# Performance work log

Measured on AMD Instinct MI355X. Metric: run time of the kernel, lower is better.

## Reference

```python
import jax, jax.numpy as jnp
import numpy as np

DN = ('NCDHW', 'OIDHW', 'NCDHW')  # torch Conv3d layout

def conv3d(x, w, b, pad):
    y = jax.lax.conv_general_dilated(x, w, (1, 1, 1), [(p, p) for p in pad], dimension_numbers=DN)
    return y + b[None, :, None, None, None]

def setup_inputs() -> dict:
    key = jax.random.key(0)
    ks = jax.random.split(key, 10)
    C, Cq = 64, 8  # in_channels, in_channels // 8
    s = 0.05
    x = jax.random.normal(ks[0], (2, C, 16, 16, 16), dtype=jnp.float32)
    return {
        'x': x,
        'wq': jax.random.normal(ks[1], (Cq, C, 1, 3, 1), jnp.float32) * s,
        'bq': jax.random.normal(ks[2], (Cq,), jnp.float32) * s,
        'wk': jax.random.normal(ks[3], (Cq, C, 3, 1, 1), jnp.float32) * s,
        'bk': jax.random.normal(ks[4], (Cq,), jnp.float32) * s,
        'wj': jax.random.normal(ks[5], (Cq, C, 1, 1, 3), jnp.float32) * s,
        'bj': jax.random.normal(ks[6], (Cq,), jnp.float32) * s,
        'wv': jax.random.normal(ks[7], (C, C, 1, 1, 1), jnp.float32) * s,
        'bv': jax.random.normal(ks[8], (C,), jnp.float32) * s,
        'gamma': jax.random.normal(ks[9], (1,), jnp.float32) * s,
    }

def reference(x, wq, bq, wk, bk, wj, bj, wv, bv, gamma):
    B, C, H, W, D = x.shape
    N = H * W * D
    q = conv3d(x, wq, bq, (0, 1, 0)).reshape(B, -1, N)   # [B, c, N]
    k = conv3d(x, wk, bk, (1, 0, 0)).reshape(B, -1, N)   # [B, c, N]
    j = conv3d(x, wj, bj, (0, 0, 1)).reshape(B, -1, N)   # [B, c, N]
    # affinity = (Q^T K) (J^T K) reassociated as Q^T (K J^T) K  -- identical math,
    # O(N^2 c) instead of O(N^3) since c = C//8 << N.
    kj = jnp.einsum('bcn,bdn->bcd', k, j)                # [B, c, c] = K @ J^T
    aff = jnp.einsum('bcn,bcd,bdm->bnm', q, kj, k)       # [B, N, N]
    aff = jax.nn.softmax(aff, axis=-1)
    v = conv3d(x, wv, bv, (0, 0, 0)).reshape(B, C, N)    # [B, C, N]
    weights = jnp.einsum('bcn,bnm->bcm', v, aff).reshape(B, C, H, W, D)
    return gamma * weights + x
```

## Files before the change

### kernel.cpp

```cpp
#include <hip/hip_runtime.h>

#define N 4096
#define CIN 64
#define NB 2

typedef unsigned short u16;
typedef short bf16x8 __attribute__((ext_vector_type(8)));
typedef float f32x4 __attribute__((ext_vector_type(4)));

#define OFF_QT 0
#define OFF_KT (OFF_QT + NB*N*8)
#define OFF_JT (OFF_KT + NB*N*8)
#define OFF_V  (OFF_JT + NB*N*8)
#define OFF_QK (OFF_V + NB*CIN*N)
#define OFF_MX (OFF_QK + NB*N*8)
#define OFF_SC (OFF_MX + NB*N)

__device__ __forceinline__ u16 f2bf(float f) {
    union { float f; unsigned u; } v; v.f = f;
    unsigned r = (v.u + 0x7fffu + ((v.u >> 16) & 1u)) >> 16;
    return (u16)r;
}

__global__ __launch_bounds__(256) void prep(
        const float* __restrict__ x,
        const float* __restrict__ wq, const float* __restrict__ bq,
        const float* __restrict__ wk, const float* __restrict__ bk,
        const float* __restrict__ wj, const float* __restrict__ bj,
        const float* __restrict__ wv, const float* __restrict__ bv,
        float* __restrict__ ws, u16* __restrict__ vbf, float* __restrict__ out) {
    int n = blockIdx.x * 256 + threadIdx.x;
    int y = blockIdx.y;
    int b = blockIdx.z;
    const float* xb = x + (size_t)b * CIN * N + n;

    if (y < 8) {
        int cq = y;
        int d = n & 15, w = (n >> 4) & 15, h = n >> 8;
        int owl = (w > 0) ? -16 : 0,  owh = (w < 15) ? 16 : 0;
        int ohl = (h > 0) ? -256 : 0, ohh = (h < 15) ? 256 : 0;
        int odl = (d > 0) ? -1 : 0,   odh = (d < 15) ? 1 : 0;
        float mwl = (w > 0) ? 1.f : 0.f, mwh = (w < 15) ? 1.f : 0.f;
        float mhl = (h > 0) ? 1.f : 0.f, mhh = (h < 15) ? 1.f : 0.f;
        float mdl = (d > 0) ? 1.f : 0.f, mdh = (d < 15) ? 1.f : 0.f;
        float q = bq[cq], k = bk[cq], j = bj[cq];
        for (int c0 = 0; c0 < CIN; c0 += 8) {
            float xc[8], xwl[8], xwh[8], xhl[8], xhh[8], xdl[8], xdh[8];
#pragma unroll
            for (int u = 0; u < 8; ++u) {
                const float* p = xb + (size_t)(c0 + u) * N;
                xc[u]  = p[0];
                xwl[u] = p[owl]; xwh[u] = p[owh];
                xhl[u] = p[ohl]; xhh[u] = p[ohh];
                xdl[u] = p[odl]; xdh[u] = p[odh];
            }
#pragma unroll
            for (int u = 0; u < 8; ++u) {
                int c = c0 + u;
                const float* wqr = wq + (cq * CIN + c) * 3;
                const float* wkr = wk + (cq * CIN + c) * 3;
                const float* wjr = wj + (cq * CIN + c) * 3;
                q += wqr[0] * (xwl[u] * mwl) + wqr[1] * xc[u] + wqr[2] * (xwh[u] * mwh);
                k += wkr[0] * (xhl[u] * mhl) + wkr[1] * xc[u] + wkr[2] * (xhh[u] * mhh);
                j += wjr[0] * (xdl[u] * mdl) + wjr[1] * xc[u] + wjr[2] * (xdh[u] * mdh);
            }
        }
        size_t base = (size_t)(b * N + n) * 8 + cq;
        ws[OFF_QT + base] = q;
        ws[OFF_KT + base] = k;
        ws[OFF_JT + base] = j;
    } else {
        int yy = y - 8;
        int co0 = yy * 8;
        float acc[8];
#pragma unroll
        for (int i = 0; i < 8; ++i) acc[i] = bv[co0 + i];
        for (int c0 = 0; c0 < CIN; c0 += 8) {
            float xv[8];
#pragma unroll
            for (int u = 0; u < 8; ++u) xv[u] = xb[(size_t)(c0 + u) * N];
#pragma unroll
            for (int u = 0; u < 8; ++u)
#pragma unroll
                for (int i = 0; i < 8; ++i)
                    acc[i] += wv[(co0 + i) * CIN + c0 + u] * xv[u];
            if ((c0 >> 3) == yy) {
#pragma unroll
                for (int u = 0; u < 8; ++u)
                    out[(size_t)(b * CIN + c0 + u) * N + n] = xv[u];
            }
        }
#pragma unroll
        for (int i = 0; i < 8; ++i)
            vbf[(size_t)(b * CIN + co0 + i) * N + n] = f2bf(acc[i]);
    }
}

__global__ __launch_bounds__(256) void kjqkj(const float* __restrict__ ws_in,
                                             float* __restrict__ ws) {
    __shared__ float kjpart[4][64];
    __shared__ float kjs[64];
    const int t = threadIdx.x, lane = t & 63, wid = t >> 6;
    const int b = blockIdx.y;
    const float* ktb = ws_in + OFF_KT + (size_t)b * N * 8;
    const float* jtb = ws_in + OFF_JT + (size_t)b * N * 8;
    const float* qtb = ws_in + OFF_QT + (size_t)b * N * 8;

    float acc[64];
#pragma unroll
    for (int i = 0; i < 64; ++i) acc[i] = 0.f;
    for (int i = 0; i < 16; ++i) {
        int nn = i * 256 + t;
        const float4* kt = (const float4*)(ktb + (size_t)nn * 8);
        const float4* jt = (const float4*)(jtb + (size_t)nn * 8);
        float4 ka = kt[0], kb = kt[1], ja = jt[0], jb = jt[1];
        float kv[8] = {ka.x, ka.y, ka.z, ka.w, kb.x, kb.y, kb.z, kb.w};
        float jv[8] = {ja.x, ja.y, ja.z, ja.w, jb.x, jb.y, jb.z, jb.w};
#pragma unroll
        for (int c = 0; c < 8; ++c)
#pragma unroll
            for (int dd = 0; dd < 8; ++dd) acc[c * 8 + dd] += kv[c] * jv[dd];
    }
#pragma unroll
    for (int s = 32; s >= 1; s >>= 1)
#pragma unroll
        for (int i = 0; i < 64; ++i) acc[i] += __shfl_down(acc[i], s, 64);
    if (lane == 0) {
#pragma unroll
        for (int i = 0; i < 64; ++i) kjpart[wid][i] = acc[i];
    }
    __syncthreads();
    if (t < 64) kjs[t] = kjpart[0][t] + kjpart[1][t] + kjpart[2][t] + kjpart[3][t];
    __syncthreads();

    float kjr[64];
#pragma unroll
    for (int i = 0; i < 64; ++i) kjr[i] = kjs[i];
    int m = blockIdx.x * 256 + t;
    const float4* qt = (const float4*)(qtb + (size_t)m * 8);
    float4 qa = qt[0], qb = qt[1];
    float qv[8] = {qa.x, qa.y, qa.z, qa.w, qb.x, qb.y, qb.z, qb.w};
    float o[8];
#pragma unroll
    for (int dd = 0; dd < 8; ++dd) {
        float a = 0.f;
#pragma unroll
        for (int c = 0; c < 8; ++c) a += qv[c] * kjr[c * 8 + dd];
        o[dd] = a;
    }
    float4* dst = (float4*)(ws + OFF_QK + (size_t)(b * N + m) * 8);
    dst[0] = make_float4(o[0], o[1], o[2], o[3]);
    dst[1] = make_float4(o[4], o[5], o[6], o[7]);
}

__global__ __launch_bounds__(256) void pass1(const float* __restrict__ ws,
                                             float* __restrict__ mx_o, float* __restrict__ sc_o,
                                             const float* __restrict__ gamma) {
    int wid = threadIdx.x >> 6, lane = threadIdx.x & 63;
    int gw = blockIdx.x * 4 + wid;
    int r0 = gw * 4;
    int b = r0 >> 12;
    float4 qa[4], qb[4];
#pragma unroll
    for (int rr = 0; rr < 4; ++rr) {
        const float4* q4 = (const float4*)(ws + OFF_QK + (size_t)(r0 + rr) * 8);
        qa[rr] = q4[0]; qb[rr] = q4[1];
    }
    const float* ktb = ws + OFF_KT + (size_t)b * N * 8;
    float mx[4], sm[4];
#pragma unroll
    for (int rr = 0; rr < 4; ++rr) { mx[rr] = -3.0e38f; sm[rr] = 0.f; }
#pragma unroll 4
    for (int i = 0; i < 64; ++i) {
        int m = i * 64 + lane;
        const float4* kk4 = (const float4*)(ktb + (size_t)m * 8);
        float4 ka = kk4[0], kb = kk4[1];
#pragma unroll
        for (int rr = 0; rr < 4; ++rr) {
            float a = qa[rr].x * ka.x + qa[rr].y * ka.y + qa[rr].z * ka.z + qa[rr].w * ka.w
                    + qb[rr].x * kb.x + qb[rr].y * kb.y + qb[rr].z * kb.z + qb[rr].w * kb.w;
            float nm = fmaxf(mx[rr], a);
            sm[rr] = sm[rr] * __expf(mx[rr] - nm) + __expf(a - nm);
            mx[rr] = nm;
        }
    }
#pragma unroll
    for (int s = 32; s >= 1; s >>= 1)
#pragma unroll
        for (int rr = 0; rr < 4; ++rr) {
            float omx = __shfl_xor(mx[rr], s, 64);
            float osm = __shfl_xor(sm[rr], s, 64);
            float nm = fmaxf(mx[rr], omx);
            sm[rr] = sm[rr] * __expf(mx[rr] - nm) + osm * __expf(omx - nm);
            mx[rr] = nm;
        }
    if (lane == 0) {
        float g = gamma[0];
#pragma unroll
        for (int rr = 0; rr < 4; ++rr) {
            mx_o[r0 + rr] = mx[rr];
            sc_o[r0 + rr] = g / sm[rr];
        }
    }
}

__global__ __launch_bounds__(256) void pass2(const float* __restrict__ ws,
                                             const u16* __restrict__ vbf,
                                             float* __restrict__ out) {
    __shared__ u16 Pt[64][72];
    __shared__ u16 Vt[64][72];
    __shared__ float ks[64][8];
    const int t  = threadIdx.x;
    const int b  = blockIdx.z;
    const int m0 = blockIdx.x * 64;
    const int ns = blockIdx.y;
    const float* qkT = ws + OFF_QK + (size_t)b * N * 8;
    const float* ktb = ws + OFF_KT + (size_t)b * N * 8;
    const float* mxv = ws + OFF_MX + (size_t)b * N;
    const float* scv = ws + OFF_SC + (size_t)b * N;
    const u16*   vb  = vbf + (size_t)b * CIN * N;

    if (t < 128) ((float4*)ks)[t] = ((const float4*)(ktb + (size_t)m0 * 8))[t];

    const int lane = t & 63;
    const int wid  = t >> 6;
    const int l16  = lane & 15;
    const int lq   = lane >> 4;
    const int vc   = t >> 3;
    const int vseg = t & 7;

    f32x4 acc[4];
#pragma unroll
    for (int i = 0; i < 4; ++i) acc[i] = (f32x4){0.f, 0.f, 0.f, 0.f};

    for (int ch = 0; ch < 8; ++ch) {
        const int n0 = ns * 512 + ch * 64;
        const int n  = n0 + lane;
        const float4* q4 = (const float4*)(qkT + (size_t)n * 8);
        float4 qa = q4[0], qb = q4[1];
        float mxl = mxv[n], sl = scv[n];
        uint4 v0 = *(const uint4*)(vb + (size_t)vc        * N + n0 + vseg * 8);
        uint4 v1 = *(const uint4*)(vb + (size_t)(vc + 32) * N + n0 + vseg * 8);
        __syncthreads();
#pragma unroll
        for (int r = 0; r < 16; ++r) {
            int mi = wid * 16 + r;
            float4 k0 = *(const float4*)&ks[mi][0];
            float4 k1 = *(const float4*)&ks[mi][4];
            float a = qa.x * k0.x + qa.y * k0.y + qa.z * k0.z + qa.w * k0.w
                    + qb.x * k1.x + qb.y * k1.y + qb.z * k1.z + qb.w * k1.w;
            Pt[mi][lane] = f2bf(__expf(a - mxl) * sl);
        }
        *(uint4*)&Vt[vc][vseg * 8]      = v0;
        *(uint4*)&Vt[vc + 32][vseg * 8] = v1;
        __syncthreads();
#pragma unroll
        for (int kk = 0; kk < 2; ++kk) {
            int k0i = kk * 32 + lq * 8;
            bf16x8 bfrag = *(const bf16x8*)&Pt[wid * 16 + l16][k0i];
#pragma unroll
            for (int ct = 0; ct < 4; ++ct) {
                bf16x8 afrag = *(const bf16x8*)&Vt[ct * 16 + l16][k0i];
                acc[ct] = __builtin_amdgcn_mfma_f32_16x16x32_bf16(afrag, bfrag, acc[ct], 0, 0, 0);
            }
        }
    }
    float* ob = out + (size_t)b * CIN * N;
    const int mcol = m0 + wid * 16 + l16;
#pragma unroll
    for (int ct = 0; ct < 4; ++ct)
#pragma unroll
        for (int r = 0; r < 4; ++r) {
            int c = ct * 16 + lq * 4 + r;
            atomicAdd(&ob[(size_t)c * N + mcol], acc[ct][r]);
        }
}

extern "C" void kernel_launch(void* const* d_in, const int* in_sizes, int n_in,
                              void* d_out, int out_size, void* d_ws, size_t ws_size,
                              hipStream_t stream) {
    const float* x  = (const float*)d_in[0];
    const float* wq = (const float*)d_in[1];
    const float* bq = (const float*)d_in[2];
    const float* wk = (const float*)d_in[3];
    const float* bk = (const float*)d_in[4];
    const float* wj = (const float*)d_in[5];
    const float* bj = (const float*)d_in[6];
    const float* wv = (const float*)d_in[7];
    const float* bv = (const float*)d_in[8];
    const float* gamma = (const float*)d_in[9];
    float* ws  = (float*)d_ws;
    float* out = (float*)d_out;
    u16* vbf = (u16*)(ws + OFF_V);

    prep<<<dim3(16, 16, 2), 256, 0, stream>>>(x, wq, bq, wk, bk, wj, bj, wv, bv, ws, vbf, out);
    kjqkj<<<dim3(16, 2), 256, 0, stream>>>(ws, ws);
    pass1<<<512, 256, 0, stream>>>(ws, ws + OFF_MX, ws + OFF_SC, gamma);
    pass2<<<dim3(64, 8, 2), 256, 0, stream>>>(ws, vbf, out);
}
```

Measured before the change: 154.7 us.

## Fuse four kernels into one persistent kernel with grid barriers

Merges prep, kj/qkj, softmax-stats and the PV pass into a single 512-block kernel. The stages are separated by atomic-counter grid barriers, which are reset with a memset before each launch. The final pass now uses 4 n-splits of 1024 instead of 8 of 512, so the grid matches 512 blocks and there are fewer output atomics. This removes three launch gaps, but it relies on all 512 blocks being co-resident (launch_bounds 256,2), and a spin barrier can deadlock or be slow if they are not. The kj stage runs on only 32 blocks while the others sit at the barrier.

```diff
diff --git a/kernel.cpp b/kernel.cpp
--- a/kernel.cpp
+++ b/kernel.cpp
@@ -3,6 +3,7 @@
 #define N 4096
 #define CIN 64
 #define NB 2
+#define NBLK 512
 
 typedef unsigned short u16;
 typedef short bf16x8 __attribute__((ext_vector_type(8)));
@@ -15,6 +16,7 @@
 #define OFF_QK (OFF_V + NB*CIN*N)
 #define OFF_MX (OFF_QK + NB*N*8)
 #define OFF_SC (OFF_MX + NB*N)
+#define OFF_CTR (OFF_SC + NB*N)
 
 __device__ __forceinline__ u16 f2bf(float f) {
     union { float f; unsigned u; } v; v.f = f;
@@ -22,258 +24,273 @@
     return (u16)r;
 }
 
-__global__ __launch_bounds__(256) void prep(
+__device__ __forceinline__ void gridbar(unsigned* ctr) {
+    __syncthreads();
+    if (threadIdx.x == 0) {
+        __threadfence();
+        atomicAdd(ctr, 1u);
+        int guard = 0;
+        while (atomicAdd(ctr, 0u) < (unsigned)NBLK && guard < (1 << 24)) {
+            __builtin_amdgcn_s_sleep(2);
+            ++guard;
+        }
+        __threadfence();
+    }
+    __syncthreads();
+}
+
+__global__ __launch_bounds__(256, 2) void fused(
         const float* __restrict__ x,
         const float* __restrict__ wq, const float* __restrict__ bq,
         const float* __restrict__ wk, const float* __restrict__ bk,
         const float* __restrict__ wj, const float* __restrict__ bj,
         const float* __restrict__ wv, const float* __restrict__ bv,
-        float* __restrict__ ws, u16* __restrict__ vbf, float* __restrict__ out) {
-    int n = blockIdx.x * 256 + threadIdx.x;
-    int y = blockIdx.y;
-    int b = blockIdx.z;
-    const float* xb = x + (size_t)b * CIN * N + n;
-
-    if (y < 8) {
-        int cq = y;
-        int d = n & 15, w = (n >> 4) & 15, h = n >> 8;
-        int owl = (w > 0) ? -16 : 0,  owh = (w < 15) ? 16 : 0;
-        int ohl = (h > 0) ? -256 : 0, ohh = (h < 15) ? 256 : 0;
-        int odl = (d > 0) ? -1 : 0,   odh = (d < 15) ? 1 : 0;
-        float mwl = (w > 0) ? 1.f : 0.f, mwh = (w < 15) ? 1.f : 0.f;
-        float mhl = (h > 0) ? 1.f : 0.f, mhh = (h < 15) ? 1.f : 0.f;
-        float mdl = (d > 0) ? 1.f : 0.f, mdh = (d < 15) ? 1.f : 0.f;
-        float q = bq[cq], k = bk[cq], j = bj[cq];
-        for (int c0 = 0; c0 < CIN; c0 += 8) {
-            float xc[8], xwl[8], xwh[8], xhl[8], xhh[8], xdl[8], xdh[8];
-#pragma unroll
-            for (int u = 0; u < 8; ++u) {
-                const float* p = xb + (size_t)(c0 + u) * N;
-                xc[u]  = p[0];
-                xwl[u] = p[owl]; xwh[u] = p[owh];
-                xhl[u] = p[ohl]; xhh[u] = p[ohh];
-                xdl[u] = p[odl]; xdh[u] = p[odh];
-            }
-#pragma unroll
-            for (int u = 0; u < 8; ++u) {
-                int c = c0 + u;
-                const float* wqr = wq + (cq * CIN + c) * 3;
-                const float* wkr = wk + (cq * CIN + c) * 3;
-                const float* wjr = wj + (cq * CIN + c) * 3;
-                q += wqr[0] * (xwl[u] * mwl) + wqr[1] * xc[u] + wqr[2] * (xwh[u] * mwh);
-                k += wkr[0] * (xhl[u] * mhl) + wkr[1] * xc[u] + wkr[2] * (xhh[u] * mhh);
-                j += wjr[0] * (xdl[u] * mdl) + wjr[1] * xc[u] + wjr[2] * (xdh[u] * mdh);
-            }
-        }
-        size_t base = (size_t)(b * N + n) * 8 + cq;
-        ws[OFF_QT + base] = q;
-        ws[OFF_KT + base] = k;
-        ws[OFF_JT + base] = j;
-    } else {
-        int yy = y - 8;
-        int co0 = yy * 8;
-        float acc[8];
-#pragma unroll
-        for (int i = 0; i < 8; ++i) acc[i] = bv[co0 + i];
-        for (int c0 = 0; c0 < CIN; c0 += 8) {
-            float xv[8];
-#pragma unroll
-            for (int u = 0; u < 8; ++u) xv[u] = xb[(size_t)(c0 + u) * N];
-#pragma unroll
-            for (int u = 0; u < 8; ++u)
-#pragma unroll
-                for (int i = 0; i < 8; ++i)
-                    acc[i] += wv[(co0 + i) * CIN + c0 + u] * xv[u];
-            if ((c0 >> 3) == yy) {
+        const float* __restrict__ gamma,
+        float* __restrict__ ws, float* __restrict__ out) {
+    const int t   = threadIdx.x;
+    const int gid = blockIdx.x;
+    u16* vbf = (u16*)(ws + OFF_V);
+    unsigned* ctr = (unsigned*)(ws + OFF_CTR);
+
+    __shared__ union {
+        struct { u16 Pt[64][72]; u16 Vt[64][72]; float ks[64][8]; } p5;
+        struct { float kjpart[4][64]; float kjs[64]; } p3;
+    } sm;
+
+    {
+        int bi = gid & 15, y = (gid >> 4) & 15, b = gid >> 8;
+        int n = bi * 256 + t;
+        const float* xb = x + (size_t)b * CIN * N + n;
+        if (y < 8) {
+            int cq = y;
+            int d = n & 15, w = (n >> 4) & 15, h = n >> 8;
+            int owl = (w > 0) ? -16 : 0,  owh = (w < 15) ? 16 : 0;
+            int ohl = (h > 0) ? -256 : 0, ohh = (h < 15) ? 256 : 0;
+            int odl = (d > 0) ? -1 : 0,   odh = (d < 15) ? 1 : 0;
+            float mwl = (w > 0) ? 1.f : 0.f, mwh = (w < 15) ? 1.f : 0.f;
+            float mhl = (h > 0) ? 1.f : 0.f, mhh = (h < 15) ? 1.f : 0.f;
+            float mdl = (d > 0) ? 1.f : 0.f, mdh = (d < 15) ? 1.f : 0.f;
+            float q = bq[cq], k = bk[cq], j = bj[cq];
+            for (int c0 = 0; c0 < CIN; c0 += 8) {
+                float xc[8], xwl[8], xwh[8], xhl[8], xhh[8], xdl[8], xdh[8];
+#pragma unroll
+                for (int u = 0; u < 8; ++u) {
+                    const float* p = xb + (size_t)(c0 + u) * N;
+                    xc[u]  = p[0];
+                    xwl[u] = p[owl]; xwh[u] = p[owh];
+                    xhl[u] = p[ohl]; xhh[u] = p[ohh];
+                    xdl[u] = p[odl]; xdh[u] = p[odh];
+                }
+#pragma unroll
+                for (int u = 0; u < 8; ++u) {
+                    int c = c0 + u;
+                    const float* wqr = wq + (cq * CIN + c) * 3;
+                    const float* wkr = wk + (cq * CIN + c) * 3;
+                    const float* wjr = wj + (cq * CIN + c) * 3;
+                    q += wqr[0] * (xwl[u] * mwl) + wqr[1] * xc[u] + wqr[2] * (xwh[u] * mwh);
+                    k += wkr[0] * (xhl[u] * mhl) + wkr[1] * xc[u] + wkr[2] * (xhh[u] * mhh);
+                    j += wjr[0] * (xdl[u] * mdl) + wjr[1] * xc[u] + wjr[2] * (xdh[u] * mdh);
+                }
+            }
+            size_t base = (size_t)(b * N + n) * 8 + cq;
+            ws[OFF_QT + base] = q;
+            ws[OFF_KT + base] = k;
+            ws[OFF_JT + base] = j;
+        } else {
+            int yy = y - 8;
+            int co0 = yy * 8;
+            float acc[8];
+#pragma unroll
+            for (int i = 0; i < 8; ++i) acc[i] = bv[co0 + i];
+            for (int c0 = 0; c0 < CIN; c0 += 8) {
+                float xv[8];
+#pragma unroll
+                for (int u = 0; u < 8; ++u) xv[u] = xb[(size_t)(c0 + u) * N];
 #pragma unroll
                 for (int u = 0; u < 8; ++u)
-                    out[(size_t)(b * CIN + c0 + u) * N + n] = xv[u];
-            }
-        }
-#pragma unroll
-        for (int i = 0; i < 8; ++i)
-            vbf[(size_t)(b * CIN + co0 + i) * N + n] = f2bf(acc[i]);
-    }
-}
-
-__global__ __launch_bounds__(256) void kjqkj(const float* __restrict__ ws_in,
-                                             float* __restrict__ ws) {
-    __shared__ float kjpart[4][64];
-    __shared__ float kjs[64];
-    const int t = threadIdx.x, lane = t & 63, wid = t >> 6;
-    const int b = blockIdx.y;
-    const float* ktb = ws_in + OFF_KT + (size_t)b * N * 8;
-    const float* jtb = ws_in + OFF_JT + (size_t)b * N * 8;
-    const float* qtb = ws_in + OFF_QT + (size_t)b * N * 8;
-
-    float acc[64];
-#pragma unroll
-    for (int i = 0; i < 64; ++i) acc[i] = 0.f;
-    for (int i = 0; i < 16; ++i) {
-        int nn = i * 256 + t;
-        const float4* kt = (const float4*)(ktb + (size_t)nn * 8);
-        const float4* jt = (const float4*)(jtb + (size_t)nn * 8);
-        float4 ka = kt[0], kb = kt[1], ja = jt[0], jb = jt[1];
-        float kv[8] = {ka.x, ka.y, ka.z, ka.w, kb.x, kb.y, kb.z, kb.w};
-        float jv[8] = {ja.x, ja.y, ja.z, ja.w, jb.x, jb.y, jb.z, jb.w};
-#pragma unroll
-        for (int c = 0; c < 8; ++c)
-#pragma unroll
-            for (int dd = 0; dd < 8; ++dd) acc[c * 8 + dd] += kv[c] * jv[dd];
-    }
-#pragma unroll
-    for (int s = 32; s >= 1; s >>= 1)
-#pragma unroll
-        for (int i = 0; i < 64; ++i) acc[i] += __shfl_down(acc[i], s, 64);
-    if (lane == 0) {
-#pragma unroll
-        for (int i = 0; i < 64; ++i) kjpart[wid][i] = acc[i];
-    }
-    __syncthreads();
-    if (t < 64) kjs[t] = kjpart[0][t] + kjpart[1][t] + kjpart[2][t] + kjpart[3][t];
-    __syncthreads();
-
-    float kjr[64];
-#pragma unroll
-    for (int i = 0; i < 64; ++i) kjr[i] = kjs[i];
-    int m = blockIdx.x * 256 + t;
-    const float4* qt = (const float4*)(qtb + (size_t)m * 8);
-    float4 qa = qt[0], qb = qt[1];
-    float qv[8] = {qa.x, qa.y, qa.z, qa.w, qb.x, qb.y, qb.z, qb.w};
-    float o[8];
-#pragma unroll
-    for (int dd = 0; dd < 8; ++dd) {
-        float a = 0.f;
-#pragma unroll
-        for (int c = 0; c < 8; ++c) a += qv[c] * kjr[c * 8 + dd];
-        o[dd] = a;
-    }
-    float4* dst = (float4*)(ws + OFF_QK + (size_t)(b * N + m) * 8);
-    dst[0] = make_float4(o[0], o[1], o[2], o[3]);
-    dst[1] = make_float4(o[4], o[5], o[6], o[7]);
-}
-
-__global__ __launch_bounds__(256) void pass1(const float* __restrict__ ws,
-                                             float* __restrict__ mx_o, float* __restrict__ sc_o,
-                                             const float* __restrict__ gamma) {
-    int wid = threadIdx.x >> 6, lane = threadIdx.x & 63;
-    int gw = blockIdx.x * 4 + wid;
-    int r0 = gw * 4;
-    int b = r0 >> 12;
-    float4 qa[4], qb[4];
-#pragma unroll
-    for (int rr = 0; rr < 4; ++rr) {
-        const float4* q4 = (const float4*)(ws + OFF_QK + (size_t)(r0 + rr) * 8);
-        qa[rr] = q4[0]; qb[rr] = q4[1];
-    }
-    const float* ktb = ws + OFF_KT + (size_t)b * N * 8;
-    float mx[4], sm[4];
-#pragma unroll
-    for (int rr = 0; rr < 4; ++rr) { mx[rr] = -3.0e38f; sm[rr] = 0.f; }
+#pragma unroll
+                    for (int i = 0; i < 8; ++i)
+                        acc[i] += wv[(co0 + i) * CIN + c0 + u] * xv[u];
+                if ((c0 >> 3) == yy) {
+#pragma unroll
+                    for (int u = 0; u < 8; ++u)
+                        out[(size_t)(b * CIN + c0 + u) * N + n] = xv[u];
+                }
+            }
+#pragma unroll
+            for (int i = 0; i < 8; ++i)
+                vbf[(size_t)(b * CIN + co0 + i) * N + n] = f2bf(acc[i]);
+        }
+    }
+    gridbar(ctr + 0);
+
+    if (gid < 32) {
+        const int lane = t & 63, wid = t >> 6;
+        const int b = gid >> 4, mblk = gid & 15;
+        const float* ktb = ws + OFF_KT + (size_t)b * N * 8;
+        const float* jtb = ws + OFF_JT + (size_t)b * N * 8;
+        const float* qtb = ws + OFF_QT + (size_t)b * N * 8;
+        float acc[64];
+#pragma unroll
+        for (int i = 0; i < 64; ++i) acc[i] = 0.f;
+        for (int i = 0; i < 16; ++i) {
+            int nn = i * 256 + t;
+            const float4* kt = (const float4*)(ktb + (size_t)nn * 8);
+            const float4* jt = (const float4*)(jtb + (size_t)nn * 8);
+            float4 ka = kt[0], kb = kt[1], ja = jt[0], jb = jt[1];
+            float kv[8] = {ka.x, ka.y, ka.z, ka.w, kb.x, kb.y, kb.z, kb.w};
+            float jv[8] = {ja.x, ja.y, ja.z, ja.w, jb.x, jb.y, jb.z, jb.w};
+#pragma unroll
+            for (int c = 0; c < 8; ++c)
+#pragma unroll
+                for (int dd = 0; dd < 8; ++dd) acc[c * 8 + dd] += kv[c] * jv[dd];
+        }
+#pragma unroll
+        for (int s = 32; s >= 1; s >>= 1)
+#pragma unroll
+            for (int i = 0; i < 64; ++i) acc[i] += __shfl_down(acc[i], s, 64);
+        if (lane == 0) {
+#pragma unroll
+            for (int i = 0; i < 64; ++i) sm.p3.kjpart[wid][i] = acc[i];
+        }
+        __syncthreads();
+        if (t < 64) sm.p3.kjs[t] = sm.p3.kjpart[0][t] + sm.p3.kjpart[1][t]
+                                 + sm.p3.kjpart[2][t] + sm.p3.kjpart[3][t];
+        __syncthreads();
+        float kjr[64];
+#pragma unroll
+        for (int i = 0; i < 64; ++i) kjr[i] = sm.p3.kjs[i];
+        int m = mblk * 256 + t;
+        const float4* qt = (const float4*)(qtb + (size_t)m * 8);
+        float4 qa = qt[0], qb = qt[1];
+        float qv[8] = {qa.x, qa.y, qa.z, qa.w, qb.x, qb.y, qb.z, qb.w};
+        float o[8];
+#pragma unroll
+        for (int dd = 0; dd < 8; ++dd) {
+            float a = 0.f;
+#pragma unroll
+            for (int c = 0; c < 8; ++c) a += qv[c] * kjr[c * 8 + dd];
+            o[dd] = a;
+        }
+        float4* dst = (float4*)(ws + OFF_QK + (size_t)(b * N + m) * 8);
+        dst[0] = make_float4(o[0], o[1], o[2], o[3]);
+        dst[1] = make_float4(o[4], o[5], o[6], o[7]);
+    }
+    gridbar(ctr + 1);
+
+    {
+        int wid = t >> 6, lane = t & 63;
+        int r0 = (gid * 4 + wid) * 4;
+        int b = r0 >> 12;
+        float4 qa[4], qb[4];
+#pragma unroll
+        for (int rr = 0; rr < 4; ++rr) {
+            const float4* q4 = (const float4*)(ws + OFF_QK + (size_t)(r0 + rr) * 8);
+            qa[rr] = q4[0]; qb[rr] = q4[1];
+        }
+        const float* ktb = ws + OFF_KT + (size_t)b * N * 8;
+        float mx[4], smv[4];
+#pragma unroll
+        for (int rr = 0; rr < 4; ++rr) { mx[rr] = -3.0e38f; smv[rr] = 0.f; }
 #pragma unroll 4
-    for (int i = 0; i < 64; ++i) {
-        int m = i * 64 + lane;
-        const float4* kk4 = (const float4*)(ktb + (size_t)m * 8);
-        float4 ka = kk4[0], kb = kk4[1];
-#pragma unroll
-        for (int rr = 0; rr < 4; ++rr) {
-            float a = qa[rr].x * ka.x + qa[rr].y * ka.y + qa[rr].z * ka.z + qa[rr].w * ka.w
-                    + qb[rr].x * kb.x + qb[rr].y * kb.y + qb[rr].z * kb.z + qb[rr].w * kb.w;
-            float nm = fmaxf(mx[rr], a);
-            sm[rr] = sm[rr] * __expf(mx[rr] - nm) + __expf(a - nm);
-            mx[rr] = nm;
-        }
-    }
-#pragma unroll
-    for (int s = 32; s >= 1; s >>= 1)
-#pragma unroll
-        for (int rr = 0; rr < 4; ++rr) {
-            float omx = __shfl_xor(mx[rr], s, 64);
-            float osm = __shfl_xor(sm[rr], s, 64);
-            float nm = fmaxf(mx[rr], omx);
-            sm[rr] = sm[rr] * __expf(mx[rr] - nm) + osm * __expf(omx - nm);
-            mx[rr] = nm;
-        }
-    if (lane == 0) {
-        float g = gamma[0];
-#pragma unroll
-        for (int rr = 0; rr < 4; ++rr) {
-            mx_o[r0 + rr] = mx[rr];
-            sc_o[r0 + rr] = g / sm[rr];
-        }
-    }
-}
-
-__global__ __launch_bounds__(256) void pass2(const float* __restrict__ ws,
-                                             const u16* __restrict__ vbf,
-                                             float* __restrict__ out) {
-    __shared__ u16 Pt[64][72];
-    __shared__ u16 Vt[64][72];
-    __shared__ float ks[64][8];
-    const int t  = threadIdx.x;
-    const int b  = blockIdx.z;
-    const int m0 = blockIdx.x * 64;
-    const int ns = blockIdx.y;
-    const float* qkT = ws + OFF_QK + (size_t)b * N * 8;
-    const float* ktb = ws + OFF_KT + (size_t)b * N * 8;
-    const float* mxv = ws + OFF_MX + (size_t)b * N;
-    const float* scv = ws + OFF_SC + (size_t)b * N;
-    const u16*   vb  = vbf + (size_t)b * CIN * N;
-
-    if (t < 128) ((float4*)ks)[t] = ((const float4*)(ktb + (size_t)m0 * 8))[t];
-
-    const int lane = t & 63;
-    const int wid  = t >> 6;
-    const int l16  = lane & 15;
-    const int lq   = lane >> 4;
-    const int vc   = t >> 3;
-    const int vseg = t & 7;
-
-    f32x4 acc[4];
-#pragma unroll
-    for (int i = 0; i < 4; ++i) acc[i] = (f32x4){0.f, 0.f, 0.f, 0.f};
-
-    for (int ch = 0; ch < 8; ++ch) {
-        const int n0 = ns * 512 + ch * 64;
-        const int n  = n0 + lane;
-        const float4* q4 = (const float4*)(qkT + (size_t)n * 8);
-        float4 qa = q4[0], qb = q4[1];
-        float mxl = mxv[n], sl = scv[n];
-        uint4 v0 = *(const uint4*)(vb + (size_t)vc        * N + n0 + vseg * 8);
-        uint4 v1 = *(const uint4*)(vb + (size_t)(vc + 32) * N + n0 + vseg * 8);
-        __syncthreads();
-#pragma unroll
-        for (int r = 0; r < 16; ++r) {
-            int mi = wid * 16 + r;
-            float4 k0 = *(const float4*)&ks[mi][0];
-            float4 k1 = *(const float4*)&ks[mi][4];
-            float a = qa.x * k0.x + qa.y * k0.y + qa.z * k0.z + qa.w * k0.w
-                    + qb.x * k1.x + qb.y * k1.y + qb.z * k1.z + qb.w * k1.w;
-            Pt[mi][lane] = f2bf(__expf(a - mxl) * sl);
-        }
-        *(uint4*)&Vt[vc][vseg * 8]      = v0;
-        *(uint4*)&Vt[vc + 32][vseg * 8] = v1;
-        __syncthreads();
-#pragma unroll
-        for (int kk = 0; kk < 2; ++kk) {
-            int k0i = kk * 32 + lq * 8;
-            bf16x8 bfrag = *(const bf16x8*)&Pt[wid * 16 + l16][k0i];
-#pragma unroll
-            for (int ct = 0; ct < 4; ++ct) {
-                bf16x8 afrag = *(const bf16x8*)&Vt[ct * 16 + l16][k0i];
-                acc[ct] = __builtin_amdgcn_mfma_f32_16x16x32_bf16(afrag, bfrag, acc[ct], 0, 0, 0);
-            }
-        }
-    }
-    float* ob = out + (size_t)b * CIN * N;
-    const int mcol = m0 + wid * 16 + l16;
-#pragma unroll
-    for (int ct = 0; ct < 4; ++ct)
-#pragma unroll
-        for (int r = 0; r < 4; ++r) {
-            int c = ct * 16 + lq * 4 + r;
-            atomicAdd(&ob[(size_t)c * N + mcol], acc[ct][r]);
-        }
+        for (int i = 0; i < 64; ++i) {
+            int m = i * 64 + lane;
+            const float4* kk4 = (const float4*)(ktb + (size_t)m * 8);
+            float4 ka = kk4[0], kb = kk4[1];
+#pragma unroll
+            for (int rr = 0; rr < 4; ++rr) {
+                float a = qa[rr].x * ka.x + qa[rr].y * ka.y + qa[rr].z * ka.z + qa[rr].w * ka.w
+                        + qb[rr].x * kb.x + qb[rr].y * kb.y + qb[rr].z * kb.z + qb[rr].w * kb.w;
+                float nm = fmaxf(mx[rr], a);
+                smv[rr] = smv[rr] * __expf(mx[rr] - nm) + __expf(a - nm);
+                mx[rr] = nm;
+            }
+        }
+#pragma unroll
+        for (int s = 32; s >= 1; s >>= 1)
+#pragma unroll
+            for (int rr = 0; rr < 4; ++rr) {
+                float omx = __shfl_xor(mx[rr], s, 64);
+                float osm = __shfl_xor(smv[rr], s, 64);
+                float nm = fmaxf(mx[rr], omx);
+                smv[rr] = smv[rr] * __expf(mx[rr] - nm) + osm * __expf(omx - nm);
+                mx[rr] = nm;
+            }
+        if (lane == 0) {
+            float g = gamma[0];
+#pragma unroll
+            for (int rr = 0; rr < 4; ++rr) {
+                ws[OFF_MX + r0 + rr] = mx[rr];
+                ws[OFF_SC + r0 + rr] = g / smv[rr];
+            }
+        }
+    }
+    gridbar(ctr + 2);
+
+    {
+        const int mt = gid & 63, ns = (gid >> 6) & 3, b = gid >> 8;
+        const int m0 = mt * 64;
+        const float* qkT = ws + OFF_QK + (size_t)b * N * 8;
+        const float* ktb = ws + OFF_KT + (size_t)b * N * 8;
+        const float* mxv = ws + OFF_MX + (size_t)b * N;
+        const float* scv = ws + OFF_SC + (size_t)b * N;
+        const u16*   vb  = vbf + (size_t)b * CIN * N;
+
+        if (t < 128) ((float4*)sm.p5.ks)[t] = ((const float4*)(ktb + (size_t)m0 * 8))[t];
+
+        const int lane = t & 63;
+        const int wid  = t >> 6;
+        const int l16  = lane & 15;
+        const int lq   = lane >> 4;
+        const int vc   = t >> 3;
+        const int vseg = t & 7;
+
+        f32x4 acc[4];
+#pragma unroll
+        for (int i = 0; i < 4; ++i) acc[i] = (f32x4){0.f, 0.f, 0.f, 0.f};
+
+        for (int ch = 0; ch < 16; ++ch) {
+            const int n0 = ns * 1024 + ch * 64;
+            const int n  = n0 + lane;
+            const float4* q4 = (const float4*)(qkT + (size_t)n * 8);
+            float4 qa = q4[0], qb = q4[1];
+            float mxl = mxv[n], sl = scv[n];
+            uint4 v0 = *(const uint4*)(vb + (size_t)vc        * N + n0 + vseg * 8);
+            uint4 v1 = *(const uint4*)(vb + (size_t)(vc + 32) * N + n0 + vseg * 8);
+            __syncthreads();
+#pragma unroll
+            for (int r = 0; r < 16; ++r) {
+                int mi = wid * 16 + r;
+                float4 k0 = *(const float4*)&sm.p5.ks[mi][0];
+                float4 k1 = *(const float4*)&sm.p5.ks[mi][4];
+                float a = qa.x * k0.x + qa.y * k0.y + qa.z * k0.z + qa.w * k0.w
+                        + qb.x * k1.x + qb.y * k1.y + qb.z * k1.z + qb.w * k1.w;
+                sm.p5.Pt[mi][lane] = f2bf(__expf(a - mxl) * sl);
+            }
+            *(uint4*)&sm.p5.Vt[vc][vseg * 8]      = v0;
+            *(uint4*)&sm.p5.Vt[vc + 32][vseg * 8] = v1;
+            __syncthreads();
+#pragma unroll
+            for (int kk = 0; kk < 2; ++kk) {
+                int k0i = kk * 32 + lq * 8;
+                bf16x8 bfrag = *(const bf16x8*)&sm.p5.Pt[wid * 16 + l16][k0i];
+#pragma unroll
+                for (int ct = 0; ct < 4; ++ct) {
+                    bf16x8 afrag = *(const bf16x8*)&sm.p5.Vt[ct * 16 + l16][k0i];
+                    acc[ct] = __builtin_amdgcn_mfma_f32_16x16x32_bf16(afrag, bfrag, acc[ct], 0, 0, 0);
+                }
+            }
+        }
+        float* ob = out + (size_t)b * CIN * N;
+        const int mcol = m0 + wid * 16 + l16;
+#pragma unroll
+        for (int ct = 0; ct < 4; ++ct)
+#pragma unroll
+            for (int r = 0; r < 4; ++r) {
+                int c = ct * 16 + lq * 4 + r;
+                atomicAdd(&ob[(size_t)c * N + mcol], acc[ct][r]);
+            }
+    }
 }
 
 extern "C" void kernel_launch(void* const* d_in, const int* in_sizes, int n_in,
@@ -291,10 +308,8 @@
     const float* gamma = (const float*)d_in[9];
     float* ws  = (float*)d_ws;
     float* out = (float*)d_out;
-    u16* vbf = (u16*)(ws + OFF_V);
-
-    prep<<<dim3(16, 16, 2), 256, 0, stream>>>(x, wq, bq, wk, bk, wj, bj, wv, bv, ws, vbf, out);
-    kjqkj<<<dim3(16, 2), 256, 0, stream>>>(ws, ws);
-    pass1<<<512, 256, 0, stream>>>(ws, ws + OFF_MX, ws + OFF_SC, gamma);
-    pass2<<<dim3(64, 8, 2), 256, 0, stream>>>(ws, vbf, out);
+
+    hipMemsetAsync(ws + OFF_CTR, 0, 16, stream);
+    fused<<<dim3(NBLK), dim3(256), 0, stream>>>(x, wq, bq, wk, bk, wj, bj,
+                                                wv, bv, gamma, ws, out);
 }
```

New measurement: 299.5 us. +93.6%, slower.
